# Performance work log

Hardware: AMD Instinct MI355X
Metric: run time of the kernel (lower is better)

The kernel has to match this reference:

```python
import jax, jax.numpy as jnp
import numpy as np

NUM_USERS = 100000
NUM_ITEMS = 50000
NUM_NODES = NUM_USERS + NUM_ITEMS
EMB = 64
NUM_EDGES = 2000000
BATCH = 16384


def setup_inputs() -> dict:
    key = jax.random.key(0)
    ks = jax.random.split(key, 9)

    def xavier(k, shape):
        fan_in, fan_out = shape[-2], shape[-1]
        lim = float(np.sqrt(6.0 / (fan_in + fan_out)))
        return jax.random.uniform(k, shape, jnp.float32, -lim, lim)

    user_table = xavier(ks[0], (NUM_USERS, EMB))
    item_table = xavier(ks[1], (NUM_ITEMS, EMB))
    # gat1: in=64, heads=4, out=64 -> W1 [64, 256]; a1 [4, 128]
    W1 = xavier(ks[2], (EMB, EMB * 4))
    a1 = xavier(ks[3], (4, 2 * EMB))
    # gat2: in=256, heads=1, out=64 -> W2 [256, 64]; a2 [1, 128]
    W2 = xavier(ks[4], (EMB * 4, EMB))
    a2 = xavier(ks[5], (1, 2 * EMB))

    edge_index = jax.random.randint(ks[6], (2, NUM_EDGES), 0, NUM_NODES, dtype=jnp.int32)
    user_ids = jax.random.randint(ks[7], (BATCH,), 0, NUM_USERS, dtype=jnp.int32)
    item_ids = jax.random.randint(ks[8], (BATCH,), 0, NUM_ITEMS, dtype=jnp.int32)
    return {
        "user_table": user_table, "item_table": item_table,
        "W1": W1, "a1": a1, "W2": W2, "a2": a2,
        "edge_index": edge_index, "user_ids": user_ids, "item_ids": item_ids,
    }


def gat_layer(x, W, a, num_heads, out_features, src, dst, concat):
    n = x.shape[0]
    h = (x @ W).reshape(n, num_heads, out_features)          # [N,H,F]
    # attention score: (cat(h_src,h_dst) * a).sum(-1) == h_src.a_l + h_dst.a_r
    a_l, a_r = a[:, :out_features], a[:, out_features:]
    e_src = jnp.einsum('nhf,hf->nh', h, a_l)                 # [N,H]
    e_dst = jnp.einsum('nhf,hf->nh', h, a_r)
    att = e_src[src] + e_dst[dst]                            # [E,H]
    att = jnp.where(att > 0, att, 0.2 * att)                 # LeakyReLU(0.2)
    att = jnp.exp(att - jnp.max(att))                        # global max, as in torch code
    att_sum = jax.ops.segment_sum(att, dst, num_segments=n)  # [N,H]
    att = att / (att_sum[dst] + 1e-8)
    msg = att[:, :, None] * h[src]                           # [E,H,F]
    out = jax.ops.segment_sum(msg, dst, num_segments=n)      # [N,H,F]
    return out.reshape(n, -1) if concat else out.mean(axis=1)


def reference(user_table, item_table, W1, a1, W2, a2, edge_index, user_ids, item_ids):
    src, dst = edge_index[0], edge_index[1]
    all_emb = jnp.concatenate([user_table, item_table], axis=0)  # [N,64]
    h = gat_layer(all_emb, W1, a1, 4, EMB, src, dst, concat=True)  # [N,256]
    h = jax.nn.elu(h)
    h = gat_layer(h, W2, a2, 1, EMB, src, dst, concat=False)       # [N,64]
    h = h + all_emb
    user_emb = h[:NUM_USERS]
    item_emb = h[NUM_USERS:]
    return jnp.sum(user_emb[user_ids] * item_emb[item_ids], axis=1)
```

## Files before the change

kernel.cpp:

```cpp
#include <hip/hip_runtime.h>
#include <cstdint>
#include <cstddef>

#define NUM_USERS 100000
#define NUM_ITEMS 50000
#define NUM_NODES 150000
#define NUM_EDGES 2000000
#define BATCH 16384
#define BSHIFT 8
#define NBUCK ((NUM_NODES + 255) >> BSHIFT)
#define PA_EDGES 8192
#define PA_BLOCKS ((NUM_EDGES + PA_EDGES - 1) / PA_EDGES)

__global__ void flag_kernel(const int* __restrict__ uid, const int* __restrict__ iid,
                            int* __restrict__ nodelist, int* __restrict__ bcnt) {
  int i = blockIdx.x * blockDim.x + threadIdx.x;
  if (i < NBUCK) bcnt[i] = 0;
  if (i < BATCH) {
    nodelist[2 * i] = uid[i];
    nodelist[2 * i + 1] = NUM_USERS + iid[i];
  }
}

__global__ __launch_bounds__(256) void bhist_kernel(const int* __restrict__ dst,
                                                    int* __restrict__ bcnt) {
  __shared__ int bh[NBUCK];
  int t = threadIdx.x;
  for (int u = t; u < NBUCK; u += 256) bh[u] = 0;
  __syncthreads();
  int base = blockIdx.x * PA_EDGES;
#pragma unroll
  for (int u = 0; u < PA_EDGES / 256; ++u) {
    int e = base + u * 256 + t;
    if (e < NUM_EDGES) atomicAdd(&bh[dst[e] >> BSHIFT], 1);
  }
  __syncthreads();
  for (int u = t; u < NBUCK; u += 256) {
    int v = bh[u];
    if (v) atomicAdd(&bcnt[u], v);
  }
}

__global__ void bscan_kernel(const int* __restrict__ bcnt, int* __restrict__ bbase,
                             int* __restrict__ bcursor, int* __restrict__ offsets) {
  __shared__ int sh[1024];
  int t = threadIdx.x;
  int v = (t < NBUCK) ? bcnt[t] : 0;
  sh[t] = v;
  __syncthreads();
  for (int off = 1; off < 1024; off <<= 1) {
    int x = (t >= off) ? sh[t - off] : 0;
    __syncthreads();
    sh[t] += x;
    __syncthreads();
  }
  if (t < NBUCK) {
    bbase[t] = sh[t] - v;
    bcursor[t] = sh[t] - v;
  }
  if (t == NBUCK - 1) {
    bbase[NBUCK] = sh[t];
    offsets[NUM_NODES] = sh[t];
  }
}

__global__ __launch_bounds__(256) void bpart_kernel(const int* __restrict__ src,
                                                    const int* __restrict__ dst,
                                                    int* __restrict__ bcursor,
                                                    int2* __restrict__ ebuf) {
  __shared__ int lcnt[NBUCK];
  __shared__ int lbase[NBUCK];
  int t = threadIdx.x;
  for (int u = t; u < NBUCK; u += 256) lcnt[u] = 0;
  __syncthreads();
  int base = blockIdx.x * PA_EDGES;
#pragma unroll
  for (int u = 0; u < PA_EDGES / 256; ++u) {
    int e = base + u * 256 + t;
    if (e < NUM_EDGES) atomicAdd(&lcnt[dst[e] >> BSHIFT], 1);
  }
  __syncthreads();
  for (int u = t; u < NBUCK; u += 256) {
    int v = lcnt[u];
    lbase[u] = v ? atomicAdd(&bcursor[u], v) : 0;
    lcnt[u] = 0;
  }
  __syncthreads();
#pragma unroll
  for (int u = 0; u < PA_EDGES / 256; ++u) {
    int e = base + u * 256 + t;
    if (e < NUM_EDGES) {
      int d = dst[e];
      int b = d >> BSHIFT;
      int p = lbase[b] + atomicAdd(&lcnt[b], 1);
      ebuf[p] = make_int2(src[e], d);
    }
  }
}

__global__ __launch_bounds__(256) void bcsr_kernel(const int2* __restrict__ ebuf,
                                                   const int* __restrict__ bbase,
                                                   int* __restrict__ offsets,
                                                   int* __restrict__ srcs) {
  __shared__ int ncnt[256];
  __shared__ int sh[256];
  __shared__ int lcur[256];
  int b = blockIdx.x;
  int t = threadIdx.x;
  int node0 = b << BSHIFT;
  int ebeg = bbase[b], eend = bbase[b + 1];
  ncnt[t] = 0;
  __syncthreads();
  for (int i = ebeg + t; i < eend; i += 256)
    atomicAdd(&ncnt[ebuf[i].y - node0], 1);
  __syncthreads();
  int v = ncnt[t];
  sh[t] = v;
  __syncthreads();
  for (int off = 1; off < 256; off <<= 1) {
    int x = (t >= off) ? sh[t - off] : 0;
    __syncthreads();
    sh[t] += x;
    __syncthreads();
  }
  int excl = ebeg + sh[t] - v;
  if (node0 + t < NUM_NODES) offsets[node0 + t] = excl;
  lcur[t] = excl;
  __syncthreads();
  for (int i = ebeg + t; i < eend; i += 256) {
    int2 ed = ebuf[i];
    int p = atomicAdd(&lcur[ed.y - node0], 1);
    srcs[p] = ed.x;
  }
}

__global__ void proj1_kernel(const float* __restrict__ W1, const float* __restrict__ a1,
                             float* __restrict__ w1a, float* __restrict__ w1b) {
  int t = threadIdx.x;
  int h = t >> 6, k = t & 63;
  float sa = 0.f, sb = 0.f;
  for (int f = 0; f < 64; ++f) {
    float w = W1[(size_t)k * 256 + h * 64 + f];
    sa += w * a1[h * 128 + f];
    sb += w * a1[h * 128 + 64 + f];
  }
  w1a[h * 64 + k] = sa;
  w1b[h * 64 + k] = sb;
}

__global__ __launch_bounds__(256) void e1_kernel(
    const float* __restrict__ ut, const float* __restrict__ it,
    const float* __restrict__ w1a, const float* __restrict__ w1b,
    float* __restrict__ e1s, float* __restrict__ e1d) {
  int wid = threadIdx.x >> 6, lane = threadIdx.x & 63;
  int node = blockIdx.x * 4 + wid;
  if (node >= NUM_NODES) return;
  const float* x = (node < NUM_USERS) ? ut + (size_t)node * 64
                                      : it + (size_t)(node - NUM_USERS) * 64;
  float xv = x[lane];
#pragma unroll
  for (int h = 0; h < 4; ++h) {
    float ps = xv * w1a[h * 64 + lane];
    float pd = xv * w1b[h * 64 + lane];
#pragma unroll
    for (int off = 32; off; off >>= 1) {
      ps += __shfl_xor(ps, off, 64);
      pd += __shfl_xor(pd, off, 64);
    }
    if (lane == 0) {
      e1s[(size_t)node * 4 + h] = ps;
      e1d[(size_t)node * 4 + h] = pd;
    }
  }
}

__device__ __forceinline__ const float* row_ptr(int s, const float* __restrict__ ut,
                                                const float* __restrict__ it) {
  return (s < NUM_USERS) ? ut + (size_t)s * 64 : it + (size_t)(s - NUM_USERS) * 64;
}

__device__ __forceinline__ float lrexp(float x) {
  x = x > 0.f ? x : 0.2f * x;
  return __expf(x);
}

__device__ __forceinline__ float wnorm(float w) {
  float sum = w;
#pragma unroll
  for (int off = 32; off; off >>= 1) sum += __shfl_xor(sum, off, 64);
  return w * (1.f / (sum + 1e-8f));
}

__device__ __forceinline__ void fold4(float4& a) {
#pragma unroll
  for (int off = 16; off <= 32; off <<= 1) {
    a.x += __shfl_xor(a.x, off, 64);
    a.y += __shfl_xor(a.y, off, 64);
    a.z += __shfl_xor(a.z, off, 64);
    a.w += __shfl_xor(a.w, off, 64);
  }
}

__device__ __forceinline__ float elu(float x) {
  return x > 0.f ? x : (__expf(x) - 1.f);
}

template <int HC>
__global__ __launch_bounds__(256) void aggX_kernel(
    const int* __restrict__ offsets, const int* __restrict__ srcs,
    const float* __restrict__ e1s, const float* __restrict__ e1d,
    const float* __restrict__ ut, const float* __restrict__ it,
    int hbase, float* __restrict__ aggX) {
  int wid = threadIdx.x >> 6, lane = threadIdx.x & 63;
  int node = blockIdx.x * 4 + wid;
  if (node >= NUM_NODES) return;
  int beg = offsets[node], end = offsets[node + 1];
  int deg = end - beg;

  float edv0 = 0.f, edv1 = 0.f, edv2 = 0.f, edv3 = 0.f;
  edv0 = e1d[(size_t)node * 4 + hbase];
  if constexpr (HC > 1) edv1 = e1d[(size_t)node * 4 + hbase + 1];
  if constexpr (HC > 2) {
    edv2 = e1d[(size_t)node * 4 + hbase + 2];
    edv3 = e1d[(size_t)node * 4 + hbase + 3];
  }

  if (deg <= 64) {
    int s = 0;
    float w0 = 0.f, w1 = 0.f, w2 = 0.f, w3 = 0.f;
    if (lane < deg) {
      s = srcs[beg + lane];
      if constexpr (HC == 4) {
        float4 ev = *(const float4*)(e1s + (size_t)s * 4);
        w0 = lrexp(ev.x + edv0);
        w1 = lrexp(ev.y + edv1);
        w2 = lrexp(ev.z + edv2);
        w3 = lrexp(ev.w + edv3);
      } else if constexpr (HC == 2) {
        float2 ev = *(const float2*)(e1s + (size_t)s * 4 + hbase);
        w0 = lrexp(ev.x + edv0);
        w1 = lrexp(ev.y + edv1);
      } else {
        w0 = lrexp(e1s[(size_t)s * 4 + hbase] + edv0);
      }
    }
    w0 = wnorm(w0);
    if constexpr (HC > 1) w1 = wnorm(w1);
    if constexpr (HC > 2) { w2 = wnorm(w2); w3 = wnorm(w3); }

    const int g = lane >> 4, fl = lane & 15;
    float4 acc0 = make_float4(0.f, 0.f, 0.f, 0.f);
    float4 acc1 = acc0, acc2 = acc0, acc3 = acc0;
#pragma unroll 4
    for (int e = 0; e < deg; e += 4) {
      int ei = e + g;
      int sg = __shfl(s, ei, 64);
      float4 xv = *(const float4*)(row_ptr(sg, ut, it) + fl * 4);
      float wg0 = __shfl(w0, ei, 64);
      acc0.x += wg0 * xv.x; acc0.y += wg0 * xv.y;
      acc0.z += wg0 * xv.z; acc0.w += wg0 * xv.w;
      if constexpr (HC > 1) {
        float wg1 = __shfl(w1, ei, 64);
        acc1.x += wg1 * xv.x; acc1.y += wg1 * xv.y;
        acc1.z += wg1 * xv.z; acc1.w += wg1 * xv.w;
      }
      if constexpr (HC > 2) {
        float wg2 = __shfl(w2, ei, 64);
        acc2.x += wg2 * xv.x; acc2.y += wg2 * xv.y;
        acc2.z += wg2 * xv.z; acc2.w += wg2 * xv.w;
        float wg3 = __shfl(w3, ei, 64);
        acc3.x += wg3 * xv.x; acc3.y += wg3 * xv.y;
        acc3.z += wg3 * xv.z; acc3.w += wg3 * xv.w;
      }
    }
    fold4(acc0);
    if constexpr (HC > 1) fold4(acc1);
    if constexpr (HC > 2) { fold4(acc2); fold4(acc3); }

    if constexpr (HC == 4) {
      float4 o = (g == 0) ? acc0 : (g == 1) ? acc1 : (g == 2) ? acc2 : acc3;
      *(float4*)(aggX + (size_t)node * 256 + lane * 4) = o;
    } else if constexpr (HC == 2) {
      if (g < 2) {
        float4 o = (g == 0) ? acc0 : acc1;
        *(float4*)(aggX + (size_t)node * 128 + lane * 4) = o;
      }
    } else {
      if (g == 0) *(float4*)(aggX + (size_t)node * 64 + fl * 4) = acc0;
    }
  } else {
    float s0 = 0.f, s1 = 0.f, s2 = 0.f, s3 = 0.f;
    for (int e = beg + lane; e < end; e += 64) {
      int s = srcs[e];
      if constexpr (HC == 4) {
        float4 ev = *(const float4*)(e1s + (size_t)s * 4);
        s0 += lrexp(ev.x + edv0); s1 += lrexp(ev.y + edv1);
        s2 += lrexp(ev.z + edv2); s3 += lrexp(ev.w + edv3);
      } else if constexpr (HC == 2) {
        float2 ev = *(const float2*)(e1s + (size_t)s * 4 + hbase);
        s0 += lrexp(ev.x + edv0); s1 += lrexp(ev.y + edv1);
      } else {
        s0 += lrexp(e1s[(size_t)s * 4 + hbase] + edv0);
      }
    }
#pragma unroll
    for (int off = 32; off; off >>= 1) {
      s0 += __shfl_xor(s0, off, 64);
      if constexpr (HC > 1) s1 += __shfl_xor(s1, off, 64);
      if constexpr (HC > 2) {
        s2 += __shfl_xor(s2, off, 64);
        s3 += __shfl_xor(s3, off, 64);
      }
    }
    float i0 = 1.f / (s0 + 1e-8f), i1 = 1.f / (s1 + 1e-8f);
    float i2 = 1.f / (s2 + 1e-8f), i3 = 1.f / (s3 + 1e-8f);
    float a0 = 0.f, a1 = 0.f, a2 = 0.f, a3 = 0.f;
    for (int e = beg; e < end; ++e) {
      int sn = srcs[e];
      float xv = row_ptr(sn, ut, it)[lane];
      if constexpr (HC == 4) {
        float4 ev = *(const float4*)(e1s + (size_t)sn * 4);
        a0 += lrexp(ev.x + edv0) * i0 * xv;
        a1 += lrexp(ev.y + edv1) * i1 * xv;
        a2 += lrexp(ev.z + edv2) * i2 * xv;
        a3 += lrexp(ev.w + edv3) * i3 * xv;
      } else if constexpr (HC == 2) {
        float2 ev = *(const float2*)(e1s + (size_t)sn * 4 + hbase);
        a0 += lrexp(ev.x + edv0) * i0 * xv;
        a1 += lrexp(ev.y + edv1) * i1 * xv;
      } else {
        a0 += lrexp(e1s[(size_t)sn * 4 + hbase] + edv0) * i0 * xv;
      }
    }
    aggX[(size_t)node * (HC * 64) + lane] = a0;
    if constexpr (HC > 1) aggX[(size_t)node * (HC * 64) + 64 + lane] = a1;
    if constexpr (HC > 2) {
      aggX[(size_t)node * (HC * 64) + 128 + lane] = a2;
      aggX[(size_t)node * (HC * 64) + 192 + lane] = a3;
    }
  }
}

template <int HC>
__global__ __launch_bounds__(256, 3) void trans_kernel(
    const float* __restrict__ aggX, const float* __restrict__ W1,
    const float* __restrict__ W2, const float* __restrict__ a2,
    int hbase, int last, float* __restrict__ h2,
    float* __restrict__ e2s, float* __restrict__ e2d) {
  __shared__ __align__(16) float xs[64][68];
  __shared__ __align__(16) float wsm[64][68];
  const int t = threadIdx.x;
  const int rb = blockIdx.x;
  const int j = t & 15, i = t >> 4;
  const int row0 = rb * 64;

  float acc2[4][4];
#pragma unroll
  for (int r = 0; r < 4; ++r) { acc2[r][0] = 0.f; acc2[r][1] = 0.f; acc2[r][2] = 0.f; acc2[r][3] = 0.f; }
  if (hbase != 0) {
#pragma unroll
    for (int r = 0; r < 4; ++r) {
      int grow = row0 + i * 4 + r;
      if (grow < NUM_NODES) {
        float4 v = *(const float4*)(h2 + (size_t)grow * 64 + j * 4);
        acc2[r][0] = v.x; acc2[r][1] = v.y; acc2[r][2] = v.z; acc2[r][3] = v.w;
      }
    }
  }

#pragma unroll 1
  for (int h = 0; h < HC; ++h) {
    __syncthreads();
#pragma unroll
    for (int u = 0; u < 4; ++u) {
      int idx = t + u * 256, rw = idx >> 4, f4 = idx & 15;
      int grow = row0 + rw;
      float4 v = make_float4(0.f, 0.f, 0.f, 0.f);
      if (grow < NUM_NODES)
        v = *(const float4*)(aggX + (size_t)grow * (HC * 64) + h * 64 + f4 * 4);
      *(float4*)&xs[rw][f4 * 4] = v;
      *(float4*)&wsm[rw][f4 * 4] =
          *(const float4*)(W1 + (size_t)rw * 256 + (hbase + h) * 64 + f4 * 4);
    }
    __syncthreads();

    float t1[4][4] = {{0.f,0.f,0.f,0.f},{0.f,0.f,0.f,0.f},{0.f,0.f,0.f,0.f},{0.f,0.f,0.f,0.f}};
#pragma unroll 2
    for (int k4 = 0; k4 < 16; ++k4) {
      float4 a0 = *(const float4*)&xs[i * 4 + 0][k4 * 4];
      float4 a1_ = *(const float4*)&xs[i * 4 + 1][k4 * 4];
      float4 a2_ = *(const float4*)&xs[i * 4 + 2][k4 * 4];
      float4 a3 = *(const float4*)&xs[i * 4 + 3][k4 * 4];
#pragma unroll
      for (int c = 0; c < 4; ++c) {
        float4 bv = *(const float4*)&wsm[k4 * 4 + c][j * 4];
        float av0 = (&a0.x)[c], av1 = (&a1_.x)[c], av2 = (&a2_.x)[c], av3 = (&a3.x)[c];
        t1[0][0] += av0 * bv.x; t1[0][1] += av0 * bv.y; t1[0][2] += av0 * bv.z; t1[0][3] += av0 * bv.w;
        t1[1][0] += av1 * bv.x; t1[1][1] += av1 * bv.y; t1[1][2] += av1 * bv.z; t1[1][3] += av1 * bv.w;
        t1[2][0] += av2 * bv.x; t1[2][1] += av2 * bv.y; t1[2][2] += av2 * bv.z; t1[2][3] += av2 * bv.w;
        t1[3][0] += av3 * bv.x; t1[3][1] += av3 * bv.y; t1[3][2] += av3 * bv.z; t1[3][3] += av3 * bv.w;
      }
    }
    __syncthreads();

#pragma unroll
    for (int r = 0; r < 4; ++r) {
      float4 o;
      o.x = elu(t1[r][0]);
      o.y = elu(t1[r][1]);
      o.z = elu(t1[r][2]);
      o.w = elu(t1[r][3]);
      *(float4*)&xs[i * 4 + r][j * 4] = o;
    }
#pragma unroll
    for (int u = 0; u < 4; ++u) {
      int idx = t + u * 256, rw = idx >> 4, f4 = idx & 15;
      *(float4*)&wsm[rw][f4 * 4] =
          *(const float4*)(W2 + (size_t)((hbase + h) * 64 + rw) * 64 + f4 * 4);
    }
    __syncthreads();

#pragma unroll 2
    for (int k4 = 0; k4 < 16; ++k4) {
      float4 a0 = *(const float4*)&xs[i * 4 + 0][k4 * 4];
      float4 a1_ = *(const float4*)&xs[i * 4 + 1][k4 * 4];
      float4 a2_ = *(const float4*)&xs[i * 4 + 2][k4 * 4];
      float4 a3 = *(const float4*)&xs[i * 4 + 3][k4 * 4];
#pragma unroll
      for (int c = 0; c < 4; ++c) {
        float4 bv = *(const float4*)&wsm[k4 * 4 + c][j * 4];
        float av0 = (&a0.x)[c], av1 = (&a1_.x)[c], av2 = (&a2_.x)[c], av3 = (&a3.x)[c];
        acc2[0][0] += av0 * bv.x; acc2[0][1] += av0 * bv.y; acc2[0][2] += av0 * bv.z; acc2[0][3] += av0 * bv.w;
        acc2[1][0] += av1 * bv.x; acc2[1][1] += av1 * bv.y; acc2[1][2] += av1 * bv.z; acc2[1][3] += av1 * bv.w;
        acc2[2][0] += av2 * bv.x; acc2[2][1] += av2 * bv.y; acc2[2][2] += av2 * bv.z; acc2[2][3] += av2 * bv.w;
        acc2[3][0] += av3 * bv.x; acc2[3][1] += av3 * bv.y; acc2[3][2] += av3 * bv.z; acc2[3][3] += av3 * bv.w;
      }
    }
  }

#pragma unroll
  for (int r = 0; r < 4; ++r) {
    int grow = row0 + i * 4 + r;
    if (grow < NUM_NODES) {
      float4 o = make_float4(acc2[r][0], acc2[r][1], acc2[r][2], acc2[r][3]);
      *(float4*)(h2 + (size_t)grow * 64 + j * 4) = o;
    }
  }

  if (last) {
    const float4 alv = *(const float4*)(a2 + j * 4);
    const float4 arv = *(const float4*)(a2 + 64 + j * 4);
#pragma unroll
    for (int r = 0; r < 4; ++r) {
      float ps = acc2[r][0] * alv.x + acc2[r][1] * alv.y + acc2[r][2] * alv.z + acc2[r][3] * alv.w;
      float pd = acc2[r][0] * arv.x + acc2[r][1] * arv.y + acc2[r][2] * arv.z + acc2[r][3] * arv.w;
#pragma unroll
      for (int off = 1; off < 16; off <<= 1) {
        ps += __shfl_xor(ps, off, 64);
        pd += __shfl_xor(pd, off, 64);
      }
      if (j == 0) {
        int grow = row0 + i * 4 + r;
        if (grow < NUM_NODES) { e2s[grow] = ps; e2d[grow] = pd; }
      }
    }
  }
}

__global__ __launch_bounds__(256) void agg2_kernel(
    const int* __restrict__ offsets, const int* __restrict__ srcs,
    const float* __restrict__ e2s, const float* __restrict__ e2d,
    const int* __restrict__ nodelist, const float* __restrict__ h2,
    const float* __restrict__ ut, const float* __restrict__ it,
    float* __restrict__ hfin) {
  int wid = threadIdx.x >> 6, lane = threadIdx.x & 63;
  int idx = blockIdx.x * 4 + wid;
  if (idx >= 2 * BATCH) return;
  int node = nodelist[idx];
  int beg = offsets[node], end = offsets[node + 1];
  int deg = end - beg;
  float edv = e2d[node];

  if (deg <= 64) {
    int s = 0;
    float w = 0.f;
    if (lane < deg) {
      s = srcs[beg + lane];
      w = lrexp(e2s[s] + edv);
    }
    w = wnorm(w);

    const int g = lane >> 4, fl = lane & 15;
    float4 acc = make_float4(0.f, 0.f, 0.f, 0.f);
#pragma unroll 4
    for (int e = 0; e < deg; e += 4) {
      int ei = e + g;
      int sg = __shfl(s, ei, 64);
      float wg = __shfl(w, ei, 64);
      float4 hv = *(const float4*)(h2 + (size_t)sg * 64 + fl * 4);
      acc.x += wg * hv.x; acc.y += wg * hv.y; acc.z += wg * hv.z; acc.w += wg * hv.w;
    }
    fold4(acc);
    if (g == 0) {
      const float* rp = (node < NUM_USERS) ? ut + (size_t)node * 64
                                           : it + (size_t)(node - NUM_USERS) * 64;
      float4 res = *(const float4*)(rp + fl * 4);
      acc.x += res.x; acc.y += res.y; acc.z += res.z; acc.w += res.w;
      *(float4*)(hfin + (size_t)node * 64 + fl * 4) = acc;
    }
  } else {
    float psum = 0.f;
    for (int e = beg + lane; e < end; e += 64) {
      int s = srcs[e];
      psum += lrexp(e2s[s] + edv);
    }
#pragma unroll
    for (int off = 32; off; off >>= 1) psum += __shfl_xor(psum, off, 64);
    float inv = 1.f / (psum + 1e-8f);
    float acc = 0.f;
    for (int e = beg; e < end; ++e) {
      int s0 = srcs[e];
      acc += lrexp(e2s[s0] + edv) * inv * h2[(size_t)s0 * 64 + lane];
    }
    float res = (node < NUM_USERS) ? ut[(size_t)node * 64 + lane]
                                   : it[(size_t)(node - NUM_USERS) * 64 + lane];
    hfin[(size_t)node * 64 + lane] = acc + res;
  }
}

__global__ __launch_bounds__(256) void final_kernel(
    const float* __restrict__ hf, const int* __restrict__ uid,
    const int* __restrict__ iid, float* __restrict__ out) {
  int wid = threadIdx.x >> 6, lane = threadIdx.x & 63;
  int idx = blockIdx.x * 4 + wid;
  if (idx >= BATCH) return;
  int u = uid[idx], v = iid[idx];
  float a = hf[(size_t)u * 64 + lane];
  float b = hf[(size_t)(NUM_USERS + v) * 64 + lane];
  float p = a * b;
#pragma unroll
  for (int off = 32; off; off >>= 1) p += __shfl_xor(p, off, 64);
  if (lane == 0) out[idx] = p;
}

extern "C" void kernel_launch(void* const* d_in, const int* in_sizes, int n_in,
                              void* d_out, int out_size, void* d_ws, size_t ws_size,
                              hipStream_t stream) {
  const float* user_table = (const float*)d_in[0];
  const float* item_table = (const float*)d_in[1];
  const float* W1 = (const float*)d_in[2];
  const float* a1 = (const float*)d_in[3];
  const float* W2 = (const float*)d_in[4];
  const float* a2 = (const float*)d_in[5];
  const int* edge_index = (const int*)d_in[6];
  const int* user_ids = (const int*)d_in[7];
  const int* item_ids = (const int*)d_in[8];
  float* out = (float*)d_out;

  const int* src = edge_index;
  const int* dst = edge_index + NUM_EDGES;

  float* ws = (float*)d_ws;
  size_t off = 0;
  auto falloc = [&](size_t n) { float* p = ws + off; off += n; return p; };
  float* h2  = falloc((size_t)NUM_NODES * 64);
  float* e1s = falloc((size_t)NUM_NODES * 4);
  float* e1d = falloc((size_t)NUM_NODES * 4);
  float* e2s = falloc(NUM_NODES);
  float* e2d = falloc(NUM_NODES);
  float* w1a = falloc(256);
  float* w1b = falloc(256);
  int* offsets  = (int*)falloc(NUM_NODES + 1);
  int* srcs     = (int*)falloc(NUM_EDGES);
  int* nodelist = (int*)falloc(2 * BATCH);
  int* bcnt     = (int*)falloc(NBUCK);
  int* bbase    = (int*)falloc(NBUCK + 1);
  int* bcursor  = (int*)falloc(NBUCK);
  off = (off + 3) & ~(size_t)3;
  float* aggX = ws + off;
  size_t availElems = (ws_size / 4 > off) ? (ws_size / 4 - off) : 0;

  int2* ebuf = (int2*)aggX;

  int HC = 1;
  if (availElems >= (size_t)NUM_NODES * 256) HC = 4;
  else if (availElems >= (size_t)NUM_NODES * 128) HC = 2;
  float* hfin = aggX;

  const int nb4 = (NUM_NODES + 3) / 4;
  const int nb64 = (NUM_NODES + 63) / 64;

  flag_kernel<<<(BATCH + 255) / 256, 256, 0, stream>>>(user_ids, item_ids,
                                                       nodelist, bcnt);
  bhist_kernel<<<PA_BLOCKS, 256, 0, stream>>>(dst, bcnt);
  bscan_kernel<<<1, 1024, 0, stream>>>(bcnt, bbase, bcursor, offsets);
  bpart_kernel<<<PA_BLOCKS, 256, 0, stream>>>(src, dst, bcursor, ebuf);
  bcsr_kernel<<<NBUCK, 256, 0, stream>>>(ebuf, bbase, offsets, srcs);

  proj1_kernel<<<1, 256, 0, stream>>>(W1, a1, w1a, w1b);
  e1_kernel<<<nb4, 256, 0, stream>>>(user_table, item_table, w1a, w1b, e1s, e1d);

  for (int hbase = 0; hbase < 4; hbase += HC) {
    int last = (hbase + HC == 4) ? 1 : 0;
    switch (HC) {
      case 4:
        aggX_kernel<4><<<nb4, 256, 0, stream>>>(offsets, srcs, e1s, e1d,
                                                user_table, item_table, hbase, aggX);
        trans_kernel<4><<<nb64, 256, 0, stream>>>(aggX, W1, W2, a2, hbase, last,
                                                  h2, e2s, e2d);
        break;
      case 2:
        aggX_kernel<2><<<nb4, 256, 0, stream>>>(offsets, srcs, e1s, e1d,
                                                user_table, item_table, hbase, aggX);
        trans_kernel<2><<<nb64, 256, 0, stream>>>(aggX, W1, W2, a2, hbase, last,
                                                  h2, e2s, e2d);
        break;
      default:
        aggX_kernel<1><<<nb4, 256, 0, stream>>>(offsets, srcs, e1s, e1d,
                                                user_table, item_table, hbase, aggX);
        trans_kernel<1><<<nb64, 256, 0, stream>>>(aggX, W1, W2, a2, hbase, last,
                                                  h2, e2s, e2d);
        break;
    }
  }

  agg2_kernel<<<(2 * BATCH + 3) / 4, 256, 0, stream>>>(offsets, srcs, e2s, e2d,
                                                       nodelist, h2,
                                                       user_table, item_table, hfin);
  final_kernel<<<(BATCH + 3) / 4, 256, 0, stream>>>(hfin, user_ids, item_ids, out);
}
```

Measured before the change: 560.2 us.

## Replace scalar FP32 transform GEMMs with split-FP16 MFMA kernel

The per-node transform (aggX·W1 → ELU → ·W2) moves from an FFMA shared-memory GEMM to MFMA 16x16x32 f16 instructions. Accuracy is kept with a hi/lo split of each operand (3 MFMAs per product, scaled by 256). Aggregated features are stored as two half-precision arrays in a padded buffer. The runtime HC head-chunking path is removed and all four heads are always processed in one pass. The intermediate ELU tile is staged in XOR-swizzled LDS, and weights are pre-split by a small prep kernel. The risks are reduced occupancy from 64-thread blocks and a slight precision loss from the split-f16 scheme.

```diff
diff --git a/kernel.cpp b/kernel.cpp
--- a/kernel.cpp
+++ b/kernel.cpp
@@ -11,6 +11,12 @@
 #define NBUCK ((NUM_NODES + 255) >> BSHIFT)
 #define PA_EDGES 8192
 #define PA_BLOCKS ((NUM_EDGES + PA_EDGES - 1) / PA_EDGES)
+#define NNPAD 150016
+#define TBLK (NNPAD / 64)
+
+typedef _Float16 hf8 __attribute__((ext_vector_type(8)));
+typedef _Float16 hf4 __attribute__((ext_vector_type(4)));
+typedef float fx4 __attribute__((ext_vector_type(4)));
 
 __global__ void flag_kernel(const int* __restrict__ uid, const int* __restrict__ iid,
                             int* __restrict__ nodelist, int* __restrict__ bcnt) {
@@ -205,48 +211,62 @@
   return x > 0.f ? x : (__expf(x) - 1.f);
 }
 
-template <int HC>
-__global__ __launch_bounds__(256) void aggX_kernel(
+__device__ __forceinline__ void split4(float4 o, hf4& hv, hf4& lv) {
+  float a0 = o.x * 256.f, a1 = o.y * 256.f, a2 = o.z * 256.f, a3 = o.w * 256.f;
+  _Float16 h0 = (_Float16)a0, h1 = (_Float16)a1;
+  _Float16 h2 = (_Float16)a2, h3 = (_Float16)a3;
+  hv[0] = h0; hv[1] = h1; hv[2] = h2; hv[3] = h3;
+  lv[0] = (_Float16)(a0 - (float)h0);
+  lv[1] = (_Float16)(a1 - (float)h1);
+  lv[2] = (_Float16)(a2 - (float)h2);
+  lv[3] = (_Float16)(a3 - (float)h3);
+}
+
+__device__ __forceinline__ void splitstore(_Float16* __restrict__ hi,
+                                           _Float16* __restrict__ lo,
+                                           size_t idx, float v) {
+  v *= 256.f;
+  _Float16 h = (_Float16)v;
+  hi[idx] = h;
+  lo[idx] = (_Float16)(v - (float)h);
+}
+
+__global__ __launch_bounds__(256) void aggX4_kernel(
     const int* __restrict__ offsets, const int* __restrict__ srcs,
     const float* __restrict__ e1s, const float* __restrict__ e1d,
     const float* __restrict__ ut, const float* __restrict__ it,
-    int hbase, float* __restrict__ aggX) {
+    _Float16* __restrict__ aXhi, _Float16* __restrict__ aXlo) {
   int wid = threadIdx.x >> 6, lane = threadIdx.x & 63;
   int node = blockIdx.x * 4 + wid;
-  if (node >= NUM_NODES) return;
+  if (node >= NNPAD) return;
+  if (node >= NUM_NODES) {
+    *(float2*)(aXhi + (size_t)node * 256 + lane * 4) = make_float2(0.f, 0.f);
+    *(float2*)(aXlo + (size_t)node * 256 + lane * 4) = make_float2(0.f, 0.f);
+    return;
+  }
   int beg = offsets[node], end = offsets[node + 1];
   int deg = end - beg;
 
-  float edv0 = 0.f, edv1 = 0.f, edv2 = 0.f, edv3 = 0.f;
-  edv0 = e1d[(size_t)node * 4 + hbase];
-  if constexpr (HC > 1) edv1 = e1d[(size_t)node * 4 + hbase + 1];
-  if constexpr (HC > 2) {
-    edv2 = e1d[(size_t)node * 4 + hbase + 2];
-    edv3 = e1d[(size_t)node * 4 + hbase + 3];
-  }
+  float edv0 = e1d[(size_t)node * 4 + 0];
+  float edv1 = e1d[(size_t)node * 4 + 1];
+  float edv2 = e1d[(size_t)node * 4 + 2];
+  float edv3 = e1d[(size_t)node * 4 + 3];
 
   if (deg <= 64) {
     int s = 0;
     float w0 = 0.f, w1 = 0.f, w2 = 0.f, w3 = 0.f;
     if (lane < deg) {
       s = srcs[beg + lane];
-      if constexpr (HC == 4) {
-        float4 ev = *(const float4*)(e1s + (size_t)s * 4);
-        w0 = lrexp(ev.x + edv0);
-        w1 = lrexp(ev.y + edv1);
-        w2 = lrexp(ev.z + edv2);
-        w3 = lrexp(ev.w + edv3);
-      } else if constexpr (HC == 2) {
-        float2 ev = *(const float2*)(e1s + (size_t)s * 4 + hbase);
-        w0 = lrexp(ev.x + edv0);
-        w1 = lrexp(ev.y + edv1);
-      } else {
-        w0 = lrexp(e1s[(size_t)s * 4 + hbase] + edv0);
-      }
+      float4 ev = *(const float4*)(e1s + (size_t)s * 4);
+      w0 = lrexp(ev.x + edv0);
+      w1 = lrexp(ev.y + edv1);
+      w2 = lrexp(ev.z + edv2);
+      w3 = lrexp(ev.w + edv3);
     }
     w0 = wnorm(w0);
-    if constexpr (HC > 1) w1 = wnorm(w1);
-    if constexpr (HC > 2) { w2 = wnorm(w2); w3 = wnorm(w3); }
+    w1 = wnorm(w1);
+    w2 = wnorm(w2);
+    w3 = wnorm(w3);
 
     const int g = lane >> 4, fl = lane & 15;
     float4 acc0 = make_float4(0.f, 0.f, 0.f, 0.f);
@@ -259,58 +279,37 @@
       float wg0 = __shfl(w0, ei, 64);
       acc0.x += wg0 * xv.x; acc0.y += wg0 * xv.y;
       acc0.z += wg0 * xv.z; acc0.w += wg0 * xv.w;
-      if constexpr (HC > 1) {
-        float wg1 = __shfl(w1, ei, 64);
-        acc1.x += wg1 * xv.x; acc1.y += wg1 * xv.y;
-        acc1.z += wg1 * xv.z; acc1.w += wg1 * xv.w;
-      }
-      if constexpr (HC > 2) {
-        float wg2 = __shfl(w2, ei, 64);
-        acc2.x += wg2 * xv.x; acc2.y += wg2 * xv.y;
-        acc2.z += wg2 * xv.z; acc2.w += wg2 * xv.w;
-        float wg3 = __shfl(w3, ei, 64);
-        acc3.x += wg3 * xv.x; acc3.y += wg3 * xv.y;
-        acc3.z += wg3 * xv.z; acc3.w += wg3 * xv.w;
-      }
-    }
-    fold4(acc0);
-    if constexpr (HC > 1) fold4(acc1);
-    if constexpr (HC > 2) { fold4(acc2); fold4(acc3); }
-
-    if constexpr (HC == 4) {
-      float4 o = (g == 0) ? acc0 : (g == 1) ? acc1 : (g == 2) ? acc2 : acc3;
-      *(float4*)(aggX + (size_t)node * 256 + lane * 4) = o;
-    } else if constexpr (HC == 2) {
-      if (g < 2) {
-        float4 o = (g == 0) ? acc0 : acc1;
-        *(float4*)(aggX + (size_t)node * 128 + lane * 4) = o;
-      }
-    } else {
-      if (g == 0) *(float4*)(aggX + (size_t)node * 64 + fl * 4) = acc0;
-    }
+      float wg1 = __shfl(w1, ei, 64);
+      acc1.x += wg1 * xv.x; acc1.y += wg1 * xv.y;
+      acc1.z += wg1 * xv.z; acc1.w += wg1 * xv.w;
+      float wg2 = __shfl(w2, ei, 64);
+      acc2.x += wg2 * xv.x; acc2.y += wg2 * xv.y;
+      acc2.z += wg2 * xv.z; acc2.w += wg2 * xv.w;
+      float wg3 = __shfl(w3, ei, 64);
+      acc3.x += wg3 * xv.x; acc3.y += wg3 * xv.y;
+      acc3.z += wg3 * xv.z; acc3.w += wg3 * xv.w;
+    }
+    fold4(acc0); fold4(acc1); fold4(acc2); fold4(acc3);
+
+    float4 o = (g == 0) ? acc0 : (g == 1) ? acc1 : (g == 2) ? acc2 : acc3;
+    hf4 hv, lv;
+    split4(o, hv, lv);
+    *(hf4*)(aXhi + (size_t)node * 256 + lane * 4) = hv;
+    *(hf4*)(aXlo + (size_t)node * 256 + lane * 4) = lv;
   } else {
     float s0 = 0.f, s1 = 0.f, s2 = 0.f, s3 = 0.f;
     for (int e = beg + lane; e < end; e += 64) {
       int s = srcs[e];
-      if constexpr (HC == 4) {
-        float4 ev = *(const float4*)(e1s + (size_t)s * 4);
-        s0 += lrexp(ev.x + edv0); s1 += lrexp(ev.y + edv1);
-        s2 += lrexp(ev.z + edv2); s3 += lrexp(ev.w + edv3);
-      } else if constexpr (HC == 2) {
-        float2 ev = *(const float2*)(e1s + (size_t)s * 4 + hbase);
-        s0 += lrexp(ev.x + edv0); s1 += lrexp(ev.y + edv1);
-      } else {
-        s0 += lrexp(e1s[(size_t)s * 4 + hbase] + edv0);
-      }
+      float4 ev = *(const float4*)(e1s + (size_t)s * 4);
+      s0 += lrexp(ev.x + edv0); s1 += lrexp(ev.y + edv1);
+      s2 += lrexp(ev.z + edv2); s3 += lrexp(ev.w + edv3);
     }
 #pragma unroll
     for (int off = 32; off; off >>= 1) {
       s0 += __shfl_xor(s0, off, 64);
-      if constexpr (HC > 1) s1 += __shfl_xor(s1, off, 64);
-      if constexpr (HC > 2) {
-        s2 += __shfl_xor(s2, off, 64);
-        s3 += __shfl_xor(s3, off, 64);
-      }
+      s1 += __shfl_xor(s1, off, 64);
+      s2 += __shfl_xor(s2, off, 64);
+      s3 += __shfl_xor(s3, off, 64);
     }
     float i0 = 1.f / (s0 + 1e-8f), i1 = 1.f / (s1 + 1e-8f);
     float i2 = 1.f / (s2 + 1e-8f), i3 = 1.f / (s3 + 1e-8f);
@@ -318,151 +317,165 @@
     for (int e = beg; e < end; ++e) {
       int sn = srcs[e];
       float xv = row_ptr(sn, ut, it)[lane];
-      if constexpr (HC == 4) {
-        float4 ev = *(const float4*)(e1s + (size_t)sn * 4);
-        a0 += lrexp(ev.x + edv0) * i0 * xv;
-        a1 += lrexp(ev.y + edv1) * i1 * xv;
-        a2 += lrexp(ev.z + edv2) * i2 * xv;
-        a3 += lrexp(ev.w + edv3) * i3 * xv;
-      } else if constexpr (HC == 2) {
-        float2 ev = *(const float2*)(e1s + (size_t)sn * 4 + hbase);
-        a0 += lrexp(ev.x + edv0) * i0 * xv;
-        a1 += lrexp(ev.y + edv1) * i1 * xv;
-      } else {
-        a0 += lrexp(e1s[(size_t)sn * 4 + hbase] + edv0) * i0 * xv;
+      float4 ev = *(const float4*)(e1s + (size_t)sn * 4);
+      a0 += lrexp(ev.x + edv0) * i0 * xv;
+      a1 += lrexp(ev.y + edv1) * i1 * xv;
+      a2 += lrexp(ev.z + edv2) * i2 * xv;
+      a3 += lrexp(ev.w + edv3) * i3 * xv;
+    }
+    splitstore(aXhi, aXlo, (size_t)node * 256 + 0 * 64 + lane, a0);
+    splitstore(aXhi, aXlo, (size_t)node * 256 + 1 * 64 + lane, a1);
+    splitstore(aXhi, aXlo, (size_t)node * 256 + 2 * 64 + lane, a2);
+    splitstore(aXhi, aXlo, (size_t)node * 256 + 3 * 64 + lane, a3);
+  }
+}
+
+__global__ void wprep_kernel(const float* __restrict__ W1, const float* __restrict__ W2,
+                             _Float16* __restrict__ w1t_hi, _Float16* __restrict__ w1t_lo,
+                             _Float16* __restrict__ w2t_hi, _Float16* __restrict__ w2t_lo) {
+  int t = threadIdx.x;
+  int h = t >> 6, a = t & 63;
+  for (int k = 0; k < 64; ++k) {
+    float w = W1[(size_t)k * 256 + h * 64 + a] * 256.f;
+    _Float16 hi = (_Float16)w;
+    w1t_hi[(size_t)(h * 64 + a) * 64 + k] = hi;
+    w1t_lo[(size_t)(h * 64 + a) * 64 + k] = (_Float16)(w - (float)hi);
+
+    float v = W2[(size_t)(h * 64 + k) * 64 + a] * 256.f;
+    _Float16 hi2 = (_Float16)v;
+    w2t_hi[(size_t)(h * 64 + a) * 64 + k] = hi2;
+    w2t_lo[(size_t)(h * 64 + a) * 64 + k] = (_Float16)(v - (float)hi2);
+  }
+}
+
+__device__ __forceinline__ fx4 mfma3(fx4 c, hf8 ah, hf8 al, hf8 bh, hf8 bl) {
+  c = __builtin_amdgcn_mfma_f32_16x16x32_f16(ah, bh, c, 0, 0, 0);
+  c = __builtin_amdgcn_mfma_f32_16x16x32_f16(al, bh, c, 0, 0, 0);
+  c = __builtin_amdgcn_mfma_f32_16x16x32_f16(ah, bl, c, 0, 0, 0);
+  return c;
+}
+
+__global__ __launch_bounds__(64, 2) void trans_mfma_kernel(
+    const _Float16* __restrict__ aXhi, const _Float16* __restrict__ aXlo,
+    const _Float16* __restrict__ w1t_hi, const _Float16* __restrict__ w1t_lo,
+    const _Float16* __restrict__ w2t_hi, const _Float16* __restrict__ w2t_lo,
+    const float* __restrict__ a2v,
+    float* __restrict__ h2g, float* __restrict__ e2s, float* __restrict__ e2d) {
+  __shared__ __align__(16) _Float16 t1hi[64 * 64];
+  __shared__ __align__(16) _Float16 t1lo[64 * 64];
+  const int l = threadIdx.x;
+  const int lr = l & 15, lg = l >> 4;
+  const int node0 = blockIdx.x * 64;
+  const float DS = 1.52587890625e-05f;
+
+  fx4 acc2[4][4];
+#pragma unroll
+  for (int m = 0; m < 4; ++m)
+#pragma unroll
+    for (int n = 0; n < 4; ++n) acc2[m][n] = (fx4){0.f, 0.f, 0.f, 0.f};
+
+#pragma unroll 1
+  for (int h = 0; h < 4; ++h) {
+    fx4 acc1[4][4];
+#pragma unroll
+    for (int m = 0; m < 4; ++m)
+#pragma unroll
+      for (int n = 0; n < 4; ++n) acc1[m][n] = (fx4){0.f, 0.f, 0.f, 0.f};
+
+#pragma unroll
+    for (int ks = 0; ks < 2; ++ks) {
+      const int ko = ks * 32 + lg * 8;
+      hf8 wah[4], wal[4], xbh[4], xbl[4];
+#pragma unroll
+      for (int m = 0; m < 4; ++m) {
+        size_t wo = (size_t)((h * 64 + m * 16 + lr) * 64 + ko);
+        wah[m] = *(const hf8*)(w1t_hi + wo);
+        wal[m] = *(const hf8*)(w1t_lo + wo);
       }
-    }
-    aggX[(size_t)node * (HC * 64) + lane] = a0;
-    if constexpr (HC > 1) aggX[(size_t)node * (HC * 64) + 64 + lane] = a1;
-    if constexpr (HC > 2) {
-      aggX[(size_t)node * (HC * 64) + 128 + lane] = a2;
-      aggX[(size_t)node * (HC * 64) + 192 + lane] = a3;
-    }
-  }
-}
-
-template <int HC>
-__global__ __launch_bounds__(256, 3) void trans_kernel(
-    const float* __restrict__ aggX, const float* __restrict__ W1,
-    const float* __restrict__ W2, const float* __restrict__ a2,
-    int hbase, int last, float* __restrict__ h2,
-    float* __restrict__ e2s, float* __restrict__ e2d) {
-  __shared__ __align__(16) float xs[64][68];
-  __shared__ __align__(16) float wsm[64][68];
-  const int t = threadIdx.x;
-  const int rb = blockIdx.x;
-  const int j = t & 15, i = t >> 4;
-  const int row0 = rb * 64;
-
-  float acc2[4][4];
-#pragma unroll
-  for (int r = 0; r < 4; ++r) { acc2[r][0] = 0.f; acc2[r][1] = 0.f; acc2[r][2] = 0.f; acc2[r][3] = 0.f; }
-  if (hbase != 0) {
-#pragma unroll
-    for (int r = 0; r < 4; ++r) {
-      int grow = row0 + i * 4 + r;
-      if (grow < NUM_NODES) {
-        float4 v = *(const float4*)(h2 + (size_t)grow * 64 + j * 4);
-        acc2[r][0] = v.x; acc2[r][1] = v.y; acc2[r][2] = v.z; acc2[r][3] = v.w;
+#pragma unroll
+      for (int n = 0; n < 4; ++n) {
+        size_t xo = (size_t)(node0 + n * 16 + lr) * 256 + h * 64 + ko;
+        xbh[n] = *(const hf8*)(aXhi + xo);
+        xbl[n] = *(const hf8*)(aXlo + xo);
       }
-    }
-  }
-
-#pragma unroll 1
-  for (int h = 0; h < HC; ++h) {
-    __syncthreads();
-#pragma unroll
-    for (int u = 0; u < 4; ++u) {
-      int idx = t + u * 256, rw = idx >> 4, f4 = idx & 15;
-      int grow = row0 + rw;
-      float4 v = make_float4(0.f, 0.f, 0.f, 0.f);
-      if (grow < NUM_NODES)
-        v = *(const float4*)(aggX + (size_t)grow * (HC * 64) + h * 64 + f4 * 4);
-      *(float4*)&xs[rw][f4 * 4] = v;
-      *(float4*)&wsm[rw][f4 * 4] =
-          *(const float4*)(W1 + (size_t)rw * 256 + (hbase + h) * 64 + f4 * 4);
-    }
-    __syncthreads();
-
-    float t1[4][4] = {{0.f,0.f,0.f,0.f},{0.f,0.f,0.f,0.f},{0.f,0.f,0.f,0.f},{0.f,0.f,0.f,0.f}};
-#pragma unroll 2
-    for (int k4 = 0; k4 < 16; ++k4) {
-      float4 a0 = *(const float4*)&xs[i * 4 + 0][k4 * 4];
-      float4 a1_ = *(const float4*)&xs[i * 4 + 1][k4 * 4];
-      float4 a2_ = *(const float4*)&xs[i * 4 + 2][k4 * 4];
-      float4 a3 = *(const float4*)&xs[i * 4 + 3][k4 * 4];
-#pragma unroll
-      for (int c = 0; c < 4; ++c) {
-        float4 bv = *(const float4*)&wsm[k4 * 4 + c][j * 4];
-        float av0 = (&a0.x)[c], av1 = (&a1_.x)[c], av2 = (&a2_.x)[c], av3 = (&a3.x)[c];
-        t1[0][0] += av0 * bv.x; t1[0][1] += av0 * bv.y; t1[0][2] += av0 * bv.z; t1[0][3] += av0 * bv.w;
-        t1[1][0] += av1 * bv.x; t1[1][1] += av1 * bv.y; t1[1][2] += av1 * bv.z; t1[1][3] += av1 * bv.w;
-        t1[2][0] += av2 * bv.x; t1[2][1] += av2 * bv.y; t1[2][2] += av2 * bv.z; t1[2][3] += av2 * bv.w;
-        t1[3][0] += av3 * bv.x; t1[3][1] += av3 * bv.y; t1[3][2] += av3 * bv.z; t1[3][3] += av3 * bv.w;
+#pragma unroll
+      for (int m = 0; m < 4; ++m)
+#pragma unroll
+        for (int n = 0; n < 4; ++n)
+          acc1[m][n] = mfma3(acc1[m][n], wah[m], wal[m], xbh[n], xbl[n]);
+    }
+
+#pragma unroll
+    for (int m = 0; m < 4; ++m)
+#pragma unroll
+      for (int n = 0; n < 4; ++n) {
+        hf4 hv, lv;
+#pragma unroll
+        for (int r = 0; r < 4; ++r) {
+          float v = acc1[m][n][r] * DS;
+          v = elu(v) * 256.f;
+          _Float16 hi = (_Float16)v;
+          hv[r] = hi;
+          lv[r] = (_Float16)(v - (float)hi);
+        }
+        int nl = n * 16 + lr;
+        int ro = (m * 32 + lg * 8) ^ ((nl & 7) << 4);
+        *(hf4*)((char*)t1hi + nl * 128 + ro) = hv;
+        *(hf4*)((char*)t1lo + nl * 128 + ro) = lv;
       }
-    }
-    __syncthreads();
-
-#pragma unroll
-    for (int r = 0; r < 4; ++r) {
-      float4 o;
-      o.x = elu(t1[r][0]);
-      o.y = elu(t1[r][1]);
-      o.z = elu(t1[r][2]);
-      o.w = elu(t1[r][3]);
-      *(float4*)&xs[i * 4 + r][j * 4] = o;
-    }
-#pragma unroll
-    for (int u = 0; u < 4; ++u) {
-      int idx = t + u * 256, rw = idx >> 4, f4 = idx & 15;
-      *(float4*)&wsm[rw][f4 * 4] =
-          *(const float4*)(W2 + (size_t)((hbase + h) * 64 + rw) * 64 + f4 * 4);
-    }
-    __syncthreads();
-
-#pragma unroll 2
-    for (int k4 = 0; k4 < 16; ++k4) {
-      float4 a0 = *(const float4*)&xs[i * 4 + 0][k4 * 4];
-      float4 a1_ = *(const float4*)&xs[i * 4 + 1][k4 * 4];
-      float4 a2_ = *(const float4*)&xs[i * 4 + 2][k4 * 4];
-      float4 a3 = *(const float4*)&xs[i * 4 + 3][k4 * 4];
-#pragma unroll
-      for (int c = 0; c < 4; ++c) {
-        float4 bv = *(const float4*)&wsm[k4 * 4 + c][j * 4];
-        float av0 = (&a0.x)[c], av1 = (&a1_.x)[c], av2 = (&a2_.x)[c], av3 = (&a3.x)[c];
-        acc2[0][0] += av0 * bv.x; acc2[0][1] += av0 * bv.y; acc2[0][2] += av0 * bv.z; acc2[0][3] += av0 * bv.w;
-        acc2[1][0] += av1 * bv.x; acc2[1][1] += av1 * bv.y; acc2[1][2] += av1 * bv.z; acc2[1][3] += av1 * bv.w;
-        acc2[2][0] += av2 * bv.x; acc2[2][1] += av2 * bv.y; acc2[2][2] += av2 * bv.z; acc2[2][3] += av2 * bv.w;
-        acc2[3][0] += av3 * bv.x; acc2[3][1] += av3 * bv.y; acc2[3][2] += av3 * bv.z; acc2[3][3] += av3 * bv.w;
+
+#pragma unroll
+    for (int ks = 0; ks < 2; ++ks) {
+      const int ko = ks * 32 + lg * 8;
+      hf8 wah[4], wal[4], tbh[4], tbl[4];
+#pragma unroll
+      for (int m = 0; m < 4; ++m) {
+        size_t wo = (size_t)((h * 64 + m * 16 + lr) * 64 + ko);
+        wah[m] = *(const hf8*)(w2t_hi + wo);
+        wal[m] = *(const hf8*)(w2t_lo + wo);
       }
-    }
-  }
-
-#pragma unroll
-  for (int r = 0; r < 4; ++r) {
-    int grow = row0 + i * 4 + r;
-    if (grow < NUM_NODES) {
-      float4 o = make_float4(acc2[r][0], acc2[r][1], acc2[r][2], acc2[r][3]);
-      *(float4*)(h2 + (size_t)grow * 64 + j * 4) = o;
-    }
-  }
-
-  if (last) {
-    const float4 alv = *(const float4*)(a2 + j * 4);
-    const float4 arv = *(const float4*)(a2 + 64 + j * 4);
-#pragma unroll
-    for (int r = 0; r < 4; ++r) {
-      float ps = acc2[r][0] * alv.x + acc2[r][1] * alv.y + acc2[r][2] * alv.z + acc2[r][3] * alv.w;
-      float pd = acc2[r][0] * arv.x + acc2[r][1] * arv.y + acc2[r][2] * arv.z + acc2[r][3] * arv.w;
-#pragma unroll
-      for (int off = 1; off < 16; off <<= 1) {
-        ps += __shfl_xor(ps, off, 64);
-        pd += __shfl_xor(pd, off, 64);
+#pragma unroll
+      for (int n = 0; n < 4; ++n) {
+        int nl = n * 16 + lr;
+        int ro = (ks * 64 + lg * 16) ^ ((nl & 7) << 4);
+        tbh[n] = *(const hf8*)((char*)t1hi + nl * 128 + ro);
+        tbl[n] = *(const hf8*)((char*)t1lo + nl * 128 + ro);
       }
-      if (j == 0) {
-        int grow = row0 + i * 4 + r;
-        if (grow < NUM_NODES) { e2s[grow] = ps; e2d[grow] = pd; }
-      }
+#pragma unroll
+      for (int m = 0; m < 4; ++m)
+#pragma unroll
+        for (int n = 0; n < 4; ++n)
+          acc2[m][n] = mfma3(acc2[m][n], wah[m], wal[m], tbh[n], tbl[n]);
+    }
+  }
+
+  float ps[4] = {0.f, 0.f, 0.f, 0.f};
+  float pd[4] = {0.f, 0.f, 0.f, 0.f};
+#pragma unroll
+  for (int m = 0; m < 4; ++m) {
+    fx4 al = *(const fx4*)(a2v + m * 16 + lg * 4);
+    fx4 ar = *(const fx4*)(a2v + 64 + m * 16 + lg * 4);
+#pragma unroll
+    for (int n = 0; n < 4; ++n) {
+      fx4 v = acc2[m][n] * DS;
+      int node = node0 + n * 16 + lr;
+      if (node < NUM_NODES)
+        *(fx4*)(h2g + (size_t)node * 64 + m * 16 + lg * 4) = v;
+      ps[n] += v[0] * al[0] + v[1] * al[1] + v[2] * al[2] + v[3] * al[3];
+      pd[n] += v[0] * ar[0] + v[1] * ar[1] + v[2] * ar[2] + v[3] * ar[3];
+    }
+  }
+#pragma unroll
+  for (int n = 0; n < 4; ++n) {
+    float s = ps[n], d = pd[n];
+    s += __shfl_xor(s, 16, 64);
+    s += __shfl_xor(s, 32, 64);
+    d += __shfl_xor(d, 16, 64);
+    d += __shfl_xor(d, 32, 64);
+    int node = node0 + n * 16 + lr;
+    if (lg == n && node < NUM_NODES) {
+      e2s[node] = s;
+      e2d[node] = d;
     }
   }
 }
@@ -577,18 +590,17 @@
   int* bbase    = (int*)falloc(NBUCK + 1);
   int* bcursor  = (int*)falloc(NBUCK);
   off = (off + 3) & ~(size_t)3;
-  float* aggX = ws + off;
-  size_t availElems = (ws_size / 4 > off) ? (ws_size / 4 - off) : 0;
-
-  int2* ebuf = (int2*)aggX;
-
-  int HC = 1;
-  if (availElems >= (size_t)NUM_NODES * 256) HC = 4;
-  else if (availElems >= (size_t)NUM_NODES * 128) HC = 2;
-  float* hfin = aggX;
+  _Float16* aggXhi = (_Float16*)(ws + off); off += (size_t)NNPAD * 128;
+  _Float16* aggXlo = (_Float16*)(ws + off); off += (size_t)NNPAD * 128;
+
+  int2* ebuf = (int2*)aggXhi;
+  float* hfin = (float*)aggXhi;
+  _Float16* w1t_hi = (_Float16*)e1s;
+  _Float16* w1t_lo = w1t_hi + 4 * 64 * 64;
+  _Float16* w2t_hi = w1t_lo + 4 * 64 * 64;
+  _Float16* w2t_lo = w2t_hi + 4 * 64 * 64;
 
   const int nb4 = (NUM_NODES + 3) / 4;
-  const int nb64 = (NUM_NODES + 63) / 64;
 
   flag_kernel<<<(BATCH + 255) / 256, 256, 0, stream>>>(user_ids, item_ids,
                                                        nodelist, bcnt);
@@ -600,29 +612,13 @@
   proj1_kernel<<<1, 256, 0, stream>>>(W1, a1, w1a, w1b);
   e1_kernel<<<nb4, 256, 0, stream>>>(user_table, item_table, w1a, w1b, e1s, e1d);
 
-  for (int hbase = 0; hbase < 4; hbase += HC) {
-    int last = (hbase + HC == 4) ? 1 : 0;
-    switch (HC) {
-      case 4:
-        aggX_kernel<4><<<nb4, 256, 0, stream>>>(offsets, srcs, e1s, e1d,
-                                                user_table, item_table, hbase, aggX);
-        trans_kernel<4><<<nb64, 256, 0, stream>>>(aggX, W1, W2, a2, hbase, last,
-                                                  h2, e2s, e2d);
-        break;
-      case 2:
-        aggX_kernel<2><<<nb4, 256, 0, stream>>>(offsets, srcs, e1s, e1d,
-                                                user_table, item_table, hbase, aggX);
-        trans_kernel<2><<<nb64, 256, 0, stream>>>(aggX, W1, W2, a2, hbase, last,
-                                                  h2, e2s, e2d);
-        break;
-      default:
-        aggX_kernel<1><<<nb4, 256, 0, stream>>>(offsets, srcs, e1s, e1d,
-                                                user_table, item_table, hbase, aggX);
-        trans_kernel<1><<<nb64, 256, 0, stream>>>(aggX, W1, W2, a2, hbase, last,
-                                                  h2, e2s, e2d);
-        break;
-    }
-  }
+  aggX4_kernel<<<NNPAD / 4, 256, 0, stream>>>(offsets, srcs, e1s, e1d,
+                                              user_table, item_table,
+                                              aggXhi, aggXlo);
+  wprep_kernel<<<1, 256, 0, stream>>>(W1, W2, w1t_hi, w1t_lo, w2t_hi, w2t_lo);
+  trans_mfma_kernel<<<TBLK, 64, 0, stream>>>(aggXhi, aggXlo,
+                                             w1t_hi, w1t_lo, w2t_hi, w2t_lo,
+                                             a2, h2, e2s, e2d);
 
   agg2_kernel<<<(2 * BATCH + 3) / 4, 256, 0, stream>>>(offsets, srcs, e2s, e2d,
                                                        nodelist, h2,
```

Measured after the change: 526.7 us. -6.0%, faster.
